# Optimization experiments

Hardware: AMD Instinct MI355X
Metric: run time of the kernel (lower is better)

Reference implementation:

```python
import jax, jax.numpy as jnp
import numpy as np

B, N, DIM = 32, 576, 1024
H, HD = 16, 64            # head_dim = DIM // H
M = HD * 2                # rand_feat_dim = head_dim * rand_feat_dim_ratio(2) = 128
LAM = 0.1
NUM_STEP = 10
SCALE = HD ** (-0.5)


def setup_inputs() -> dict:
    key = jax.random.key(0)
    ks = jax.random.split(key, 6)
    x = jax.random.normal(ks[0], (B, N, DIM), dtype=jnp.float32)
    qkv_w = jax.random.normal(ks[1], (2 * DIM, DIM), dtype=jnp.float32) * 0.02
    proj_w = jax.random.normal(ks[2], (DIM, DIM), dtype=jnp.float32) * 0.02
    proj_b = jnp.zeros((DIM,), dtype=jnp.float32)
    rand_matrix = jax.random.normal(ks[3], (H, HD, M), dtype=jnp.float32)
    kernel = jax.random.normal(ks[4], (1, H, N, M), dtype=jnp.float32)
    learned_k = jnp.eye(2 * M, dtype=jnp.float32)
    learned_lam = jnp.ones((1,), dtype=jnp.float32)
    learned_L = jnp.ones((1,), dtype=jnp.float32)
    return {"x": x, "qkv_w": qkv_w, "proj_w": proj_w, "proj_b": proj_b,
            "rand_matrix": rand_matrix, "kernel": kernel,
            "learned_k": learned_k, "learned_lam": learned_lam,
            "learned_L": learned_L}


def _soft_thresh(z, t):
    # torch: sign(z) * GELU(|z| - t), exact (erf) GELU
    return jnp.sign(z) * jax.nn.gelu(jnp.abs(z) - t, approximate=False)


def reference(x, qkv_w, proj_w, proj_b, rand_matrix, kernel,
              learned_k, learned_lam, learned_L):
    # qkv projection (no bias), split into q and v heads: [B,H,N,HD]
    qkv = (x @ qkv_w.T).reshape(B, N, 2, H, HD)
    q = jnp.transpose(qkv[:, :, 0], (0, 2, 1, 3))
    v = jnp.transpose(qkv[:, :, 1], (0, 2, 1, 3))

    # random-feature map (Performer-style positive features)
    q = q * SCALE ** 0.5
    logits = jnp.einsum('bhnd,hdm->bhnm', q, rand_matrix)
    sqnorm = 0.5 * jnp.sum(q * q, axis=-1, keepdims=True)
    phi = jnp.exp(logits - sqnorm) / (M ** 0.5)                 # [B,H,N,M]

    # concat learned kernel features, L2-normalize over token dim (dim=-2)
    q = jnp.concatenate([phi, jnp.broadcast_to(kernel, (B, H, N, M))], axis=-1)
    nrm = jnp.linalg.norm(q, axis=-2, keepdims=True)
    q = q / jnp.maximum(nrm, 1e-12)                              # [B,H,N,2M]

    kk = jnp.einsum('bhnp,bhnq->bhpq', q, q)                     # [B,H,2M,2M]
    inp = jnp.einsum('bhnp,bhnd->bhpd', q, v)                    # [B,H,2M,HD]

    # ISTA-like unrolled solver
    L = jax.lax.stop_gradient(
        jnp.max(jnp.sum(jnp.abs(kk), axis=-1), axis=-1))[..., None, None] + 1.0
    lam_learned = learned_lam * LAM                              # [1]
    eff_L = L / learned_L                                        # [B,H,1,1]
    kk_learned = jnp.einsum('pq,bhqr,rs->bhps', learned_k, kk, learned_k)

    z = _soft_thresh(inp, lam_learned)
    for _ in range(NUM_STEP):
        z = z - (jnp.einsum('bhpq,bhqd->bhpd', kk_learned, z) - inp) / eff_L
        z = _soft_thresh(z, lam_learned / eff_L)

    out = jnp.einsum('bhnp,bhpd->bhnd', q, z)                    # [B,H,N,HD]
    out = jnp.transpose(out, (0, 2, 1, 3)).reshape(B, N, DIM)
    return out @ proj_w.T + proj_b
```

## Files before the change

### kernel.cpp

```cpp
#include <hip/hip_runtime.h>
#include <math.h>

#define NN 576
#define LAMC 0.1f
#define NUM_STEP 10

typedef unsigned short u16;
typedef __attribute__((ext_vector_type(8))) short bf16x8;
typedef __attribute__((ext_vector_type(4))) float f32x4;

__device__ __forceinline__ float bf2f(u16 u) { return __uint_as_float(((unsigned)u) << 16); }
__device__ __forceinline__ u16 f2bf(float f) {
    unsigned x = __float_as_uint(f);
    return (u16)((x + 0x7fffu + ((x >> 16) & 1u)) >> 16);
}
__device__ __forceinline__ float soft_thresh(float z, float t) {
    float a = fabsf(z) - t;
    float g = 0.5f * a * (1.0f + erff(a * 0.70710678118654752f));
    float s = (z > 0.0f) ? 1.0f : ((z < 0.0f) ? -1.0f : 0.0f);
    return s * g;
}
__device__ __forceinline__ void gload16(const u16* g, const u16* l) {
    __builtin_amdgcn_global_load_lds(
        (const __attribute__((address_space(1))) unsigned int*)(g),
        (__attribute__((address_space(3))) unsigned int*)(l), 16, 0, 0);
}

__global__ __launch_bounds__(256) void k_cvt(const float* __restrict__ in,
                                             u16* __restrict__ out, int n4) {
    const int i = blockIdx.x * 256 + threadIdx.x;
    if (i >= n4) return;
    float4 v = reinterpret_cast<const float4*>(in)[i];
    ushort4 o;
    o.x = f2bf(v.x); o.y = f2bf(v.y); o.z = f2bf(v.z); o.w = f2bf(v.w);
    reinterpret_cast<ushort4*>(out)[i] = o;
}

__global__ __launch_bounds__(256) void k_cvtT(const float* __restrict__ Lk,
                                              u16* __restrict__ LkT) {
    const int r = blockIdx.x, s = threadIdx.x;
    LkT[r * 256 + s] = f2bf(Lk[s * 256 + r]);
}

__global__ __launch_bounds__(256) void k_randT(const float* __restrict__ rand_m,
                                               u16* __restrict__ randT) {
    const int i = blockIdx.x * 256 + threadIdx.x;
    const int h = i >> 13, rem = i & 8191;
    const int m = rem >> 6, d = rem & 63;
    randT[i] = f2bf(rand_m[(size_t)h * 8192 + d * 128 + m]);
}

__device__ __forceinline__ void nt128_body(const u16* __restrict__ A, const u16* __restrict__ B,
                                           const int K, u16 (&As)[128][32], u16 (&Bs)[128][32],
                                           f32x4 (&acc)[4][4]) {
    const int tid = threadIdx.x;
    const int lane = tid & 63, wid = tid >> 6;
    const int wr = (wid >> 1) * 64, wc = (wid & 1) * 64;
    const int fr = lane & 15, kg = lane >> 4;
    for (int k0 = 0; k0 < K; k0 += 32) {
        __syncthreads();
        #pragma unroll
        for (int c = 0; c < 2; ++c) {
            const int ch = wid + c * 4;
            gload16(&A[(size_t)(ch * 16 + (lane >> 2)) * K + k0 + (lane & 3) * 8], &As[ch * 16][0]);
            gload16(&B[(size_t)(ch * 16 + (lane >> 2)) * K + k0 + (lane & 3) * 8], &Bs[ch * 16][0]);
        }
        __syncthreads();
        bf16x8 af[4], bfr[4];
        #pragma unroll
        for (int i = 0; i < 4; ++i) af[i] = *reinterpret_cast<const bf16x8*>(&As[wr + i * 16 + fr][kg * 8]);
        #pragma unroll
        for (int j = 0; j < 4; ++j) bfr[j] = *reinterpret_cast<const bf16x8*>(&Bs[wc + j * 16 + fr][kg * 8]);
        #pragma unroll
        for (int i = 0; i < 4; ++i)
            #pragma unroll
            for (int j = 0; j < 4; ++j)
                acc[i][j] = __builtin_amdgcn_mfma_f32_16x16x32_bf16(af[i], bfr[j], acc[i][j], 0, 0, 0);
    }
}

__global__ __launch_bounds__(256) void k_qkv_mfma(const u16* __restrict__ A,
                                                  const u16* __restrict__ B,
                                                  u16* __restrict__ qbf,
                                                  u16* __restrict__ vT) {
    __shared__ u16 As[128][32];
    __shared__ u16 Bs[128][32];
    const int tid = threadIdx.x;
    const int wid = tid >> 6, lane = tid & 63;
    const int wr = (wid >> 1) * 64, wc = (wid & 1) * 64;
    const int lb = (blockIdx.x & 7) * 288 + (blockIdx.x >> 3);
    const int bm = lb >> 4, bn = lb & 15;
    const int row0 = bm * 128, col0 = bn * 128;
    const int fr = lane & 15, kg = lane >> 4;
    f32x4 acc[4][4];
    #pragma unroll
    for (int i = 0; i < 4; ++i)
        #pragma unroll
        for (int j = 0; j < 4; ++j) acc[i][j] = (f32x4){0.f, 0.f, 0.f, 0.f};
    nt128_body(A + (size_t)row0 * 1024, B + (size_t)col0 * 1024, 1024, As, Bs, acc);
    const bool isQ = (col0 < 1024);
    if (isQ) {
        const float qscale = 0.35355339059327373f;
        #pragma unroll
        for (int i = 0; i < 4; ++i) {
            #pragma unroll
            for (int r = 0; r < 4; ++r) {
                const int grow = row0 + wr + i * 16 + kg * 4 + r;
                const int b = grow / NN, n = grow % NN;
                #pragma unroll
                for (int j = 0; j < 4; ++j) {
                    const int gcol = col0 + wc + j * 16 + fr;
                    const int h = gcol >> 6, d = gcol & 63;
                    qbf[(((size_t)b * 16 + h) * NN + n) * 64 + d] = f2bf(acc[i][j][r] * qscale);
                }
            }
        }
    } else {
        #pragma unroll
        for (int i = 0; i < 4; ++i) {
            const int gb = row0 + wr + i * 16 + kg * 4;
            const int b = gb / NN, n = gb % NN;
            #pragma unroll
            for (int j = 0; j < 4; ++j) {
                const int c2 = col0 + wc + j * 16 + fr - 1024;
                const int h = c2 >> 6, d = c2 & 63;
                ushort4 pk;
                pk.x = f2bf(acc[i][j][0]); pk.y = f2bf(acc[i][j][1]);
                pk.z = f2bf(acc[i][j][2]); pk.w = f2bf(acc[i][j][3]);
                *reinterpret_cast<ushort4*>(&vT[(((size_t)b * 16 + h) * 64 + d) * 576 + n]) = pk;
            }
        }
    }
}

__global__ __launch_bounds__(256) void k_phi_mfma(const u16* __restrict__ qbf,
                                                  const u16* __restrict__ randT,
                                                  u16* __restrict__ phiT,
                                                  float* __restrict__ invn) {
    __shared__ u16 Rs[128][72];
    __shared__ u16 Qs[64][72];
    __shared__ u16 Ph[128][72];
    __shared__ float sn[64];
    __shared__ float snorm[256];
    const int bh = blockIdx.x, h = bh & 15;
    const int tid = threadIdx.x, lane = tid & 63, wid = tid >> 6;
    const int fr = lane & 15, kg = lane >> 4;
    #pragma unroll
    for (int c = 0; c < 4; ++c) {
        const int i = c * 256 + tid;
        const int m = i >> 3, k8 = (i & 7) * 8;
        *reinterpret_cast<uint4*>(&Rs[m][k8]) =
            *reinterpret_cast<const uint4*>(&randT[((size_t)h * 128 + m) * 64 + k8]);
    }
    const u16* Q = qbf + (size_t)bh * 576 * 64;
    const float invM = 0.08838834764831845f;
    float accs = 0.f;
    const int m2 = tid >> 1, c0 = (tid & 1) * 32;
    for (int nc = 0; nc < 9; ++nc) {
        const int n0 = nc * 64;
        __syncthreads();
        #pragma unroll
        for (int c = 0; c < 2; ++c) {
            const int i = c * 256 + tid;
            const int r = i >> 3, k8 = (i & 7) * 8;
            *reinterpret_cast<uint4*>(&Qs[r][k8]) =
                *reinterpret_cast<const uint4*>(&Q[(size_t)(n0 + r) * 64 + k8]);
        }
        __syncthreads();
        if (tid < 64) {
            float s = 0.f;
            #pragma unroll 8
            for (int d = 0; d < 64; ++d) { float v = bf2f(Qs[tid][d]); s = fmaf(v, v, s); }
            sn[tid] = 0.5f * s;
        }
        f32x4 acc[2][4];
        #pragma unroll
        for (int i = 0; i < 2; ++i)
            #pragma unroll
            for (int j = 0; j < 4; ++j) acc[i][j] = (f32x4){0.f, 0.f, 0.f, 0.f};
        #pragma unroll
        for (int ks = 0; ks < 2; ++ks) {
            bf16x8 af[2], bq[4];
            #pragma unroll
            for (int i = 0; i < 2; ++i)
                af[i] = *reinterpret_cast<const bf16x8*>(&Rs[wid * 32 + i * 16 + fr][ks * 32 + kg * 8]);
            #pragma unroll
            for (int j = 0; j < 4; ++j)
                bq[j] = *reinterpret_cast<const bf16x8*>(&Qs[j * 16 + fr][ks * 32 + kg * 8]);
            #pragma unroll
            for (int i = 0; i < 2; ++i)
                #pragma unroll
                for (int j = 0; j < 4; ++j)
                    acc[i][j] = __builtin_amdgcn_mfma_f32_16x16x32_bf16(af[i], bq[j], acc[i][j], 0, 0, 0);
        }
        __syncthreads();
        #pragma unroll
        for (int j = 0; j < 4; ++j) {
            const int n = j * 16 + fr;
            const float sv = sn[n];
            #pragma unroll
            for (int i = 0; i < 2; ++i) {
                #pragma unroll
                for (int r = 0; r < 4; ++r) {
                    const int m = wid * 32 + i * 16 + kg * 4 + r;
                    Ph[m][n] = f2bf(expf(acc[i][j][r] - sv) * invM);
                }
            }
        }
        __syncthreads();
        #pragma unroll
        for (int c = 0; c < 4; ++c) {
            const int i = c * 256 + tid;
            const int mm = i >> 3, k8 = (i & 7) * 8;
            *reinterpret_cast<uint4*>(&phiT[((size_t)bh * 128 + mm) * 576 + n0 + k8]) =
                *reinterpret_cast<const uint4*>(&Ph[mm][k8]);
        }
        {
            float s = 0.f;
            #pragma unroll 8
            for (int t = 0; t < 32; ++t) { float v = bf2f(Ph[m2][c0 + t]); s = fmaf(v, v, s); }
            accs += s;
        }
    }
    snorm[tid] = accs;
    __syncthreads();
    if (tid < 128)
        invn[bh * 128 + tid] = 1.0f / fmaxf(sqrtf(snorm[tid * 2] + snorm[tid * 2 + 1]), 1e-12f);
}

__global__ __launch_bounds__(128) void k_kernormT(const float* __restrict__ kern,
                                                  u16* __restrict__ kerT) {
    const int h = blockIdx.x, m = threadIdx.x;
    const float* kp = kern + (size_t)h * NN * 128 + m;
    float s = 0.f;
    for (int n = 0; n < NN; ++n) { float v = kp[(size_t)n * 128]; s = fmaf(v, v, s); }
    const float inv = 1.0f / fmaxf(sqrtf(s), 1e-12f);
    u16* op = kerT + ((size_t)h * 128 + m) * 576;
    for (int n = 0; n < NN; ++n) op[n] = f2bf(kp[(size_t)n * 128] * inv);
}

__global__ __launch_bounds__(512, 2) void k_gram_fat(const u16* __restrict__ phiT,
                                                     const u16* __restrict__ kerT,
                                                     const float* __restrict__ invn,
                                                     u16* __restrict__ kkb) {
    __shared__ u16 Qs[256][32];
    const int bh = blockIdx.x, h = bh & 15;
    const int tid = threadIdx.x, lane = tid & 63, wid = tid >> 6;
    const int wr = (wid & 3) * 64, wc = (wid >> 2) * 128;
    const int fr = lane & 15, kg = lane >> 4;
    const int lrow = lane >> 2;
    const int lslot = (lane & 3) ^ ((lane >> 3) & 3);
    f32x4 acc[4][8];
    #pragma unroll
    for (int i = 0; i < 4; ++i)
        #pragma unroll
        for (int j = 0; j < 8; ++j) acc[i][j] = (f32x4){0.f, 0.f, 0.f, 0.f};
    const int rslot = (kg ^ ((fr >> 1) & 3)) * 8;
    for (int k0 = 0; k0 < 576; k0 += 32) {
        __syncthreads();
        #pragma unroll
        for (int c = 0; c < 2; ++c) {
            const int chunk = wid * 2 + c;
            const int p = chunk * 16 + lrow;
            const u16* src = (p < 128)
                ? phiT + ((size_t)bh * 128 + p) * 576 + k0 + lslot * 8
                : kerT + ((size_t)h * 128 + (p - 128)) * 576 + k0 + lslot * 8;
            gload16(src, &Qs[chunk * 16][0]);
        }
        __syncthreads();
        bf16x8 af[4], bf[8];
        #pragma unroll
        for (int i = 0; i < 4; ++i) af[i] = *reinterpret_cast<const bf16x8*>(&Qs[wr + i * 16 + fr][rslot]);
        #pragma unroll
        for (int j = 0; j < 8; ++j) bf[j] = *reinterpret_cast<const bf16x8*>(&Qs[wc + j * 16 + fr][rslot]);
        #pragma unroll
        for (int i = 0; i < 4; ++i)
            #pragma unroll
            for (int j = 0; j < 8; ++j)
                acc[i][j] = __builtin_amdgcn_mfma_f32_16x16x32_bf16(af[i], bf[j], acc[i][j], 0, 0, 0);
    }
    const float* iv = invn + bh * 128;
    u16* C = kkb + (size_t)bh * 65536;
    float sq[8];
    #pragma unroll
    for (int j = 0; j < 8; ++j) { const int q = wc + j * 16 + fr; sq[j] = (q < 128) ? iv[q] : 1.0f; }
    #pragma unroll
    for (int i = 0; i < 4; ++i)
        #pragma unroll
        for (int rr = 0; rr < 4; ++rr) {
            const int p = wr + i * 16 + kg * 4 + rr;
            const float sp = (p < 128) ? iv[p] : 1.0f;
            #pragma unroll
            for (int j = 0; j < 8; ++j)
                C[(size_t)p * 256 + wc + j * 16 + fr] = f2bf(acc[i][j][rr] * sp * sq[j]);
        }
}

__global__ __launch_bounds__(512, 2) void k_lk_fat(const u16* __restrict__ Ab, size_t sA,
                                                   const u16* __restrict__ Bb, size_t sB,
                                                   u16* __restrict__ Cb) {
    __shared__ u16 As[256][32];
    __shared__ u16 Bs[256][32];
    const int idx = blockIdx.x;
    const int tid = threadIdx.x, lane = tid & 63, wid = tid >> 6;
    const int wr = (wid & 3) * 64, wc = (wid >> 2) * 128;
    const int fr = lane & 15, kg = lane >> 4;
    const int lrow = lane >> 2;
    const int lslot = (lane & 3) ^ ((lane >> 3) & 3);
    const u16* A = Ab + (size_t)idx * sA;
    const u16* B = Bb + (size_t)idx * sB;
    f32x4 acc[4][8];
    #pragma unroll
    for (int i = 0; i < 4; ++i)
        #pragma unroll
        for (int j = 0; j < 8; ++j) acc[i][j] = (f32x4){0.f, 0.f, 0.f, 0.f};
    const int rslot = (kg ^ ((fr >> 1) & 3)) * 8;
    for (int k0 = 0; k0 < 256; k0 += 32) {
        __syncthreads();
        #pragma unroll
        for (int c = 0; c < 2; ++c) {
            const int chunk = wid * 2 + c;
            const int p = chunk * 16 + lrow;
            gload16(&A[(size_t)p * 256 + k0 + lslot * 8], &As[chunk * 16][0]);
            gload16(&B[(size_t)p * 256 + k0 + lslot * 8], &Bs[chunk * 16][0]);
        }
        __syncthreads();
        bf16x8 af[4], bf[8];
        #pragma unroll
        for (int i = 0; i < 4; ++i) af[i] = *reinterpret_cast<const bf16x8*>(&As[wr + i * 16 + fr][rslot]);
        #pragma unroll
        for (int j = 0; j < 8; ++j) bf[j] = *reinterpret_cast<const bf16x8*>(&Bs[wc + j * 16 + fr][rslot]);
        #pragma unroll
        for (int i = 0; i < 4; ++i)
            #pragma unroll
            for (int j = 0; j < 8; ++j)
                acc[i][j] = __builtin_amdgcn_mfma_f32_16x16x32_bf16(af[i], bf[j], acc[i][j], 0, 0, 0);
    }
    u16* C = Cb + (size_t)idx * 65536;
    #pragma unroll
    for (int i = 0; i < 4; ++i)
        #pragma unroll
        for (int rr = 0; rr < 4; ++rr) {
            const int p = wr + i * 16 + kg * 4 + rr;
            #pragma unroll
            for (int j = 0; j < 8; ++j)
                C[(size_t)p * 256 + wc + j * 16 + fr] = f2bf(acc[i][j][rr]);
        }
}

__global__ __launch_bounds__(256) void k_inp_mfma(const u16* __restrict__ vT,
                                                  const u16* __restrict__ phiT,
                                                  const u16* __restrict__ kerT,
                                                  const float* __restrict__ invn,
                                                  float* __restrict__ inpT) {
    __shared__ u16 As[64][40];
    __shared__ u16 Bs[256][40];
    const int bh = blockIdx.x, h = bh & 15;
    const int tid = threadIdx.x, lane = tid & 63, wid = tid >> 6;
    const int fr = lane & 15, kg = lane >> 4;
    const u16* Av = vT + (size_t)bh * 64 * 576;
    f32x4 acc[4][4];
    #pragma unroll
    for (int i = 0; i < 4; ++i)
        #pragma unroll
        for (int j = 0; j < 4; ++j) acc[i][j] = (f32x4){0.f, 0.f, 0.f, 0.f};
    for (int k0 = 0; k0 < 576; k0 += 32) {
        __syncthreads();
        { const int r = tid >> 2, k8 = (tid & 3) * 8;
          *reinterpret_cast<uint4*>(&As[r][k8]) =
              *reinterpret_cast<const uint4*>(&Av[(size_t)r * 576 + k0 + k8]); }
        #pragma unroll
        for (int c = 0; c < 4; ++c) {
            const int q = c * 256 + tid;
            const int r = q >> 2, k8 = (q & 3) * 8;
            const u16* src = (r < 128) ? phiT + ((size_t)bh * 128 + r) * 576
                                       : kerT + ((size_t)h * 128 + (r - 128)) * 576;
            *reinterpret_cast<uint4*>(&Bs[r][k8]) =
                *reinterpret_cast<const uint4*>(&src[k0 + k8]);
        }
        __syncthreads();
        bf16x8 af[4], bfr[4];
        #pragma unroll
        for (int i = 0; i < 4; ++i) af[i] = *reinterpret_cast<const bf16x8*>(&As[i * 16 + fr][kg * 8]);
        #pragma unroll
        for (int j = 0; j < 4; ++j) bfr[j] = *reinterpret_cast<const bf16x8*>(&Bs[wid * 64 + j * 16 + fr][kg * 8]);
        #pragma unroll
        for (int i = 0; i < 4; ++i)
            #pragma unroll
            for (int j = 0; j < 4; ++j)
                acc[i][j] = __builtin_amdgcn_mfma_f32_16x16x32_bf16(af[i], bfr[j], acc[i][j], 0, 0, 0);
    }
    float* O = inpT + (size_t)bh * 16384;
    float sc[4];
    #pragma unroll
    for (int j = 0; j < 4; ++j) {
        const int p = wid * 64 + j * 16 + fr;
        sc[j] = (p < 128) ? invn[bh * 128 + p] : 1.0f;
    }
    #pragma unroll
    for (int i = 0; i < 4; ++i)
        #pragma unroll
        for (int r = 0; r < 4; ++r)
            #pragma unroll
            for (int j = 0; j < 4; ++j)
                O[(size_t)(i * 16 + kg * 4 + r) * 256 + wid * 64 + j * 16 + fr] = acc[i][j][r] * sc[j];
}

__global__ __launch_bounds__(256) void k_L(const u16* __restrict__ kkb,
                                           const float* __restrict__ lL,
                                           float* __restrict__ effL) {
    const int bh = blockIdx.x;
    const u16* row = kkb + (size_t)bh * 65536 + (size_t)threadIdx.x * 256;
    float s = 0.f;
    for (int q = 0; q < 256; ++q) s += fabsf(bf2f(row[q]));
    __shared__ float red[256];
    red[threadIdx.x] = s;
    __syncthreads();
    for (int st = 128; st > 0; st >>= 1) {
        if (threadIdx.x < st) red[threadIdx.x] = fmaxf(red[threadIdx.x], red[threadIdx.x + st]);
        __syncthreads();
    }
    if (threadIdx.x == 0) effL[bh] = (red[0] + 1.0f) / lL[0];
}

__global__ __launch_bounds__(256) void k_ista_reg(const u16* __restrict__ kkl,
                                                  const float* __restrict__ inpT,
                                                  u16* __restrict__ zbf,
                                                  const float* __restrict__ effL,
                                                  const float* __restrict__ llam) {
    __shared__ u16 zs[32][256];
    const int bh = blockIdx.x >> 1, dh = blockIdx.x & 1;
    const int tid = threadIdx.x, lane = tid & 63, wid = tid >> 6;
    const int wr = wid * 64;
    const int fr = lane & 15, kg = lane >> 4;
    const u16* Kk = kkl + (size_t)bh * 65536;
    bf16x8 af[4][8];
    #pragma unroll
    for (int i = 0; i < 4; ++i) {
        const int p = wr + i * 16 + fr;
        #pragma unroll
        for (int c = 0; c < 8; ++c)
            af[i][c] = *reinterpret_cast<const bf16x8*>(&Kk[(size_t)p * 256 + c * 32 + kg * 8]);
    }
    const float* I = inpT + (size_t)bh * 16384 + (size_t)dh * 32 * 256;
    const float invL = 1.0f / effL[bh];
    const float lam = llam[0] * LAMC;
    const float thr = lam * invL;
    float4 ip[4][2];
    #pragma unroll
    for (int i = 0; i < 4; ++i) {
        const int pb = wr + i * 16 + kg * 4;
        #pragma unroll
        for (int j = 0; j < 2; ++j) {
            const int d = j * 16 + fr;
            ip[i][j] = *reinterpret_cast<const float4*>(&I[(size_t)d * 256 + pb]);
            const int pc = pb ^ ((d & 7) << 3);
            ushort4 pk;
            pk.x = f2bf(soft_thresh(ip[i][j].x, lam));
            pk.y = f2bf(soft_thresh(ip[i][j].y, lam));
            pk.z = f2bf(soft_thresh(ip[i][j].z, lam));
            pk.w = f2bf(soft_thresh(ip[i][j].w, lam));
            *reinterpret_cast<ushort4*>(&zs[d][pc]) = pk;
        }
    }
    __syncthreads();
    for (int step = 0; step < NUM_STEP; ++step) {
        f32x4 acc[4][2];
        #pragma unroll
        for (int i = 0; i < 4; ++i)
            #pragma unroll
            for (int j = 0; j < 2; ++j) acc[i][j] = (f32x4){0.f, 0.f, 0.f, 0.f};
        #pragma unroll
        for (int c = 0; c < 8; ++c) {
            bf16x8 bz[2];
            #pragma unroll
            for (int j = 0; j < 2; ++j) {
                const int d = j * 16 + fr;
                bz[j] = *reinterpret_cast<const bf16x8*>(&zs[d][(c * 32 + kg * 8) ^ ((d & 7) << 3)]);
            }
            #pragma unroll
            for (int i = 0; i < 4; ++i)
                #pragma unroll
                for (int j = 0; j < 2; ++j)
                    acc[i][j] = __builtin_amdgcn_mfma_f32_16x16x32_bf16(af[i][c], bz[j], acc[i][j], 0, 0, 0);
        }
        __syncthreads();
        #pragma unroll
        for (int i = 0; i < 4; ++i) {
            const int pb = wr + i * 16 + kg * 4;
            #pragma unroll
            for (int j = 0; j < 2; ++j) {
                const int d = j * 16 + fr;
                const int pc = pb ^ ((d & 7) << 3);
                ushort4 zo = *reinterpret_cast<const ushort4*>(&zs[d][pc]);
                ushort4 pk;
                pk.x = f2bf(soft_thresh(bf2f(zo.x) - (acc[i][j][0] - ip[i][j].x) * invL, thr));
                pk.y = f2bf(soft_thresh(bf2f(zo.y) - (acc[i][j][1] - ip[i][j].y) * invL, thr));
                pk.z = f2bf(soft_thresh(bf2f(zo.z) - (acc[i][j][2] - ip[i][j].z) * invL, thr));
                pk.w = f2bf(soft_thresh(bf2f(zo.w) - (acc[i][j][3] - ip[i][j].w) * invL, thr));
                *reinterpret_cast<ushort4*>(&zs[d][pc]) = pk;
            }
        }
        __syncthreads();
    }
    u16* Z = zbf + (size_t)bh * 16384 + (size_t)dh * 32 * 256;
    #pragma unroll
    for (int c = 0; c < 4; ++c) {
        const int i = c * 256 + tid;
        const int d = i >> 5, p8 = (i & 31) * 8;
        *reinterpret_cast<uint4*>(&Z[(size_t)d * 256 + p8]) =
            *reinterpret_cast<const uint4*>(&zs[d][p8 ^ ((d & 7) << 3)]);
    }
}

__global__ __launch_bounds__(256) void k_outpre_mfma(const u16* __restrict__ phiT,
                                                     const u16* __restrict__ kerT,
                                                     const u16* __restrict__ zbf,
                                                     const float* __restrict__ invn,
                                                     u16* __restrict__ outp) {
    __shared__ u16 Zs[64][264];
    __shared__ u16 Qt[64][264];
    __shared__ u16 Os[64][72];
    const int bh = blockIdx.x, b = bh >> 4, h = bh & 15;
    const int tid = threadIdx.x, lane = tid & 63, wid = tid >> 6;
    const int fr = lane & 15, kg = lane >> 4;
    const u16* Z = zbf + (size_t)bh * 16384;
    #pragma unroll
    for (int c = 0; c < 8; ++c) {
        const int i = c * 256 + tid;
        const int d = i >> 5, k8 = (i & 31) * 8;
        uint4 v = *reinterpret_cast<const uint4*>(&Z[(size_t)d * 256 + k8]);
        if (k8 < 128) {
            const float4 s0 = *reinterpret_cast<const float4*>(&invn[bh * 128 + k8]);
            const float4 s1 = *reinterpret_cast<const float4*>(&invn[bh * 128 + k8 + 4]);
            uint4 o;
            o.x = (unsigned)f2bf(__uint_as_float(v.x << 16) * s0.x) |
                  ((unsigned)f2bf(__uint_as_float(v.x & 0xffff0000u) * s0.y) << 16);
            o.y = (unsigned)f2bf(__uint_as_float(v.y << 16) * s0.z) |
                  ((unsigned)f2bf(__uint_as_float(v.y & 0xffff0000u) * s0.w) << 16);
            o.z = (unsigned)f2bf(__uint_as_float(v.z << 16) * s1.x) |
                  ((unsigned)f2bf(__uint_as_float(v.z & 0xffff0000u) * s1.y) << 16);
            o.w = (unsigned)f2bf(__uint_as_float(v.w << 16) * s1.z) |
                  ((unsigned)f2bf(__uint_as_float(v.w & 0xffff0000u) * s1.w) << 16);
            v = o;
        }
        *reinterpret_cast<uint4*>(&Zs[d][k8]) = v;
    }
    for (int nc = 0; nc < 9; ++nc) {
        const int n0 = nc * 64;
        __syncthreads();
        #pragma unroll
        for (int c = 0; c < 8; ++c) {
            const int i = c * 256 + tid;
            const int p = i >> 3, j8 = (i & 7) * 8;
            const u16* src = (p < 128) ? &phiT[((size_t)bh * 128 + p) * 576 + n0 + j8]
                                       : &kerT[((size_t)h * 128 + (p - 128)) * 576 + n0 + j8];
            uint4 v = *reinterpret_cast<const uint4*>(src);
            Qt[j8 + 0][p] = (u16)(v.x & 0xffffu); Qt[j8 + 1][p] = (u16)(v.x >> 16);
            Qt[j8 + 2][p] = (u16)(v.y & 0xffffu); Qt[j8 + 3][p] = (u16)(v.y >> 16);
            Qt[j8 + 4][p] = (u16)(v.z & 0xffffu); Qt[j8 + 5][p] = (u16)(v.z >> 16);
            Qt[j8 + 6][p] = (u16)(v.w & 0xffffu); Qt[j8 + 7][p] = (u16)(v.w >> 16);
        }
        __syncthreads();
        f32x4 acc[4];
        #pragma unroll
        for (int j = 0; j < 4; ++j) acc[j] = (f32x4){0.f, 0.f, 0.f, 0.f};
        #pragma unroll
        for (int ks = 0; ks < 8; ++ks) {
            bf16x8 aq = *reinterpret_cast<const bf16x8*>(&Qt[wid * 16 + fr][ks * 32 + kg * 8]);
            #pragma unroll
            for (int j = 0; j < 4; ++j) {
                bf16x8 bz = *reinterpret_cast<const bf16x8*>(&Zs[j * 16 + fr][ks * 32 + kg * 8]);
                acc[j] = __builtin_amdgcn_mfma_f32_16x16x32_bf16(aq, bz, acc[j], 0, 0, 0);
            }
        }
        __syncthreads();
        #pragma unroll
        for (int j = 0; j < 4; ++j)
            #pragma unroll
            for (int r = 0; r < 4; ++r)
                Os[wid * 16 + kg * 4 + r][j * 16 + fr] = f2bf(acc[j][r]);
        __syncthreads();
        #pragma unroll
        for (int c = 0; c < 2; ++c) {
            const int i = c * 256 + tid;
            const int nn = i >> 3, k8 = (i & 7) * 8;
            *reinterpret_cast<uint4*>(&outp[((size_t)b * NN + n0 + nn) * 1024 + h * 64 + k8]) =
                *reinterpret_cast<const uint4*>(&Os[nn][k8]);
        }
    }
}

__global__ __launch_bounds__(256) void k_proj_mfma(const u16* __restrict__ A,
                                                   const u16* __restrict__ B,
                                                   const float* __restrict__ bias,
                                                   float* __restrict__ out) {
    __shared__ u16 As[128][32];
    __shared__ u16 Bs[128][32];
    const int tid = threadIdx.x;
    const int wid = tid >> 6, lane = tid & 63;
    const int wr = (wid >> 1) * 64, wc = (wid & 1) * 64;
    const int lb = (blockIdx.x & 7) * 144 + (blockIdx.x >> 3);
    const int bm = lb >> 3, bn = lb & 7;
    const int row0 = bm * 128, col0 = bn * 128;
    const int fr = lane & 15, kg = lane >> 4;
    f32x4 acc[4][4];
    #pragma unroll
    for (int i = 0; i < 4; ++i)
        #pragma unroll
        for (int j = 0; j < 4; ++j) acc[i][j] = (f32x4){0.f, 0.f, 0.f, 0.f};
    nt128_body(A + (size_t)row0 * 1024, B + (size_t)col0 * 1024, 1024, As, Bs, acc);
    #pragma unroll
    for (int i = 0; i < 4; ++i)
        #pragma unroll
        for (int r = 0; r < 4; ++r) {
            const int grow = row0 + wr + i * 16 + kg * 4 + r;
            #pragma unroll
            for (int j = 0; j < 4; ++j) {
                const int gcol = col0 + wc + j * 16 + fr;
                out[(size_t)grow * 1024 + gcol] = acc[i][j][r] + bias[gcol];
            }
        }
}

extern "C" void kernel_launch(void* const* d_in, const int* in_sizes, int n_in,
                              void* d_out, int out_size, void* d_ws, size_t ws_size,
                              hipStream_t stream) {
    const float* x      = (const float*)d_in[0];
    const float* qkv_w  = (const float*)d_in[1];
    const float* proj_w = (const float*)d_in[2];
    const float* proj_b = (const float*)d_in[3];
    const float* rand_m = (const float*)d_in[4];
    const float* kern   = (const float*)d_in[5];
    const float* Lk     = (const float*)d_in[6];
    const float* llam   = (const float*)d_in[7];
    const float* lL     = (const float*)d_in[8];
    float* out = (float*)d_out;

    const size_t NEED = 248514560ull;
    if (ws_size < NEED) { hipMemsetAsync(d_out, 0, (size_t)out_size * 4, stream); return; }
    char* base = (char*)d_ws;
    u16*   pwb  = (u16*)  (base + 0);
    float* effL = (float*)(base + 2097152);
    u16*   Lkb  = (u16*)  (base + 2099200);
    u16*   LkTb = (u16*)  (base + 2230272);
    u16*   kerT = (u16*)  (base + 2361344);
    u16*   randT= (u16*)  (base + 4720640);
    u16*   phiT = (u16*)  (base + 4982784);
    u16*   kkb  = (u16*)  (base + 80480256);
    float* inpT = (float*)(base + 147589120);
    u16*   zbf  = (u16*)  (base + 181143552);
    float* invn = (float*)(base + 248252416);
    u16*   vT   = (u16*)  (base + 80480256);
    u16*   wb   = (u16*)  (base + 118228992);
    u16*   qbf  = (u16*)  (base + 147589120);
    u16*   xb   = (u16*)  (base + 197920768);
    u16*   tmpb = (u16*)  (base + 181143552);
    u16*   outp = (u16*)  (base + 80480256);

    k_cvt        <<<18432, 256, 0, stream>>>(x, xb, 4718592);
    k_cvt        <<<2048,  256, 0, stream>>>(qkv_w, wb, 524288);
    k_cvt        <<<1024,  256, 0, stream>>>(proj_w, pwb, 262144);
    k_cvt        <<<64,    256, 0, stream>>>(Lk, Lkb, 16384);
    k_cvtT       <<<256,   256, 0, stream>>>(Lk, LkTb);
    k_randT      <<<512,   256, 0, stream>>>(rand_m, randT);
    k_kernormT   <<<16,    128, 0, stream>>>(kern, kerT);
    k_qkv_mfma   <<<2304,  256, 0, stream>>>(xb, wb, qbf, vT);
    k_phi_mfma   <<<512,   256, 0, stream>>>(qbf, randT, phiT, invn);
    k_inp_mfma   <<<512,   256, 0, stream>>>(vT, phiT, kerT, invn, inpT);
    k_gram_fat   <<<512,   512, 0, stream>>>(phiT, kerT, invn, kkb);
    k_L          <<<512,   256, 0, stream>>>(kkb, lL, effL);
    k_lk_fat     <<<512,   512, 0, stream>>>(Lkb, 0, kkb, 65536, tmpb);
    k_lk_fat     <<<512,   512, 0, stream>>>(tmpb, 65536, LkTb, 0, kkb);
    k_ista_reg   <<<1024,  256, 0, stream>>>(kkb, inpT, zbf, effL, llam);
    k_outpre_mfma<<<512,   256, 0, stream>>>(phiT, kerT, zbf, invn, outp);
    k_proj_mfma  <<<1152,  256, 0, stream>>>(outp, pwb, proj_b, out);
}
```

Before: 610.0 us.

## Use 256x256 tiles with swizzled LDS for qkv and proj GEMMs

Replaces the 128x128-tile, 256-thread GEMM kernels for the qkv and output projections with 256x256-tile, 512-thread kernels where each wave computes a 64x128 sub-tile. LDS reads and writes now use an XOR swizzle on the k-slot to avoid bank conflicts. This is meant to raise arithmetic intensity and cut global/LDS traffic per MFMA. In exchange it uses more registers and launches fewer blocks (576 and 288), so load balance across CUs may suffer.

```diff
diff --git a/kernel.cpp b/kernel.cpp
--- a/kernel.cpp
+++ b/kernel.cpp
@@ -50,54 +50,49 @@
     randT[i] = f2bf(rand_m[(size_t)h * 8192 + d * 128 + m]);
 }
 
-__device__ __forceinline__ void nt128_body(const u16* __restrict__ A, const u16* __restrict__ B,
-                                           const int K, u16 (&As)[128][32], u16 (&Bs)[128][32],
-                                           f32x4 (&acc)[4][4]) {
-    const int tid = threadIdx.x;
-    const int lane = tid & 63, wid = tid >> 6;
-    const int wr = (wid >> 1) * 64, wc = (wid & 1) * 64;
-    const int fr = lane & 15, kg = lane >> 4;
-    for (int k0 = 0; k0 < K; k0 += 32) {
+__global__ __launch_bounds__(512, 2) void k_qkv_fat(const u16* __restrict__ A,
+                                                    const u16* __restrict__ B,
+                                                    u16* __restrict__ qbf,
+                                                    u16* __restrict__ vT) {
+    __shared__ u16 As[256][32];
+    __shared__ u16 Bs[256][32];
+    const int tid = threadIdx.x, lane = tid & 63, wid = tid >> 6;
+    const int wr = (wid & 3) * 64, wc = (wid >> 2) * 128;
+    const int fr = lane & 15, kg = lane >> 4;
+    const int lrow = lane >> 2;
+    const int lslot = (lane & 3) ^ ((lane >> 3) & 3);
+    const int lb = (blockIdx.x & 7) * 72 + (blockIdx.x >> 3);
+    const int bm = lb >> 3, bn = lb & 7;
+    const int row0 = bm * 256, col0 = bn * 256;
+    const u16* Ab = A + (size_t)row0 * 1024;
+    const u16* Bb = B + (size_t)col0 * 1024;
+    f32x4 acc[4][8];
+    #pragma unroll
+    for (int i = 0; i < 4; ++i)
+        #pragma unroll
+        for (int j = 0; j < 8; ++j) acc[i][j] = (f32x4){0.f, 0.f, 0.f, 0.f};
+    const int rslot = (kg ^ ((fr >> 1) & 3)) * 8;
+    for (int k0 = 0; k0 < 1024; k0 += 32) {
         __syncthreads();
         #pragma unroll
         for (int c = 0; c < 2; ++c) {
-            const int ch = wid + c * 4;
-            gload16(&A[(size_t)(ch * 16 + (lane >> 2)) * K + k0 + (lane & 3) * 8], &As[ch * 16][0]);
-            gload16(&B[(size_t)(ch * 16 + (lane >> 2)) * K + k0 + (lane & 3) * 8], &Bs[ch * 16][0]);
-        }
-        __syncthreads();
-        bf16x8 af[4], bfr[4];
-        #pragma unroll
-        for (int i = 0; i < 4; ++i) af[i] = *reinterpret_cast<const bf16x8*>(&As[wr + i * 16 + fr][kg * 8]);
-        #pragma unroll
-        for (int j = 0; j < 4; ++j) bfr[j] = *reinterpret_cast<const bf16x8*>(&Bs[wc + j * 16 + fr][kg * 8]);
+            const int chunk = wid * 2 + c;
+            const int p = chunk * 16 + lrow;
+            gload16(&Ab[(size_t)p * 1024 + k0 + lslot * 8], &As[chunk * 16][0]);
+            gload16(&Bb[(size_t)p * 1024 + k0 + lslot * 8], &Bs[chunk * 16][0]);
+        }
+        __syncthreads();
+        bf16x8 af[4], bf[8];
+        #pragma unroll
+        for (int i = 0; i < 4; ++i) af[i] = *reinterpret_cast<const bf16x8*>(&As[wr + i * 16 + fr][rslot]);
+        #pragma unroll
+        for (int j = 0; j < 8; ++j) bf[j] = *reinterpret_cast<const bf16x8*>(&Bs[wc + j * 16 + fr][rslot]);
         #pragma unroll
         for (int i = 0; i < 4; ++i)
             #pragma unroll
-            for (int j = 0; j < 4; ++j)
-                acc[i][j] = __builtin_amdgcn_mfma_f32_16x16x32_bf16(af[i], bfr[j], acc[i][j], 0, 0, 0);
-    }
-}
-
-__global__ __launch_bounds__(256) void k_qkv_mfma(const u16* __restrict__ A,
-                                                  const u16* __restrict__ B,
-                                                  u16* __restrict__ qbf,
-                                                  u16* __restrict__ vT) {
-    __shared__ u16 As[128][32];
-    __shared__ u16 Bs[128][32];
-    const int tid = threadIdx.x;
-    const int wid = tid >> 6, lane = tid & 63;
-    const int wr = (wid >> 1) * 64, wc = (wid & 1) * 64;
-    const int lb = (blockIdx.x & 7) * 288 + (blockIdx.x >> 3);
-    const int bm = lb >> 4, bn = lb & 15;
-    const int row0 = bm * 128, col0 = bn * 128;
-    const int fr = lane & 15, kg = lane >> 4;
-    f32x4 acc[4][4];
-    #pragma unroll
-    for (int i = 0; i < 4; ++i)
-        #pragma unroll
-        for (int j = 0; j < 4; ++j) acc[i][j] = (f32x4){0.f, 0.f, 0.f, 0.f};
-    nt128_body(A + (size_t)row0 * 1024, B + (size_t)col0 * 1024, 1024, As, Bs, acc);
+            for (int j = 0; j < 8; ++j)
+                acc[i][j] = __builtin_amdgcn_mfma_f32_16x16x32_bf16(af[i], bf[j], acc[i][j], 0, 0, 0);
+    }
     const bool isQ = (col0 < 1024);
     if (isQ) {
         const float qscale = 0.35355339059327373f;
@@ -108,7 +103,7 @@
                 const int grow = row0 + wr + i * 16 + kg * 4 + r;
                 const int b = grow / NN, n = grow % NN;
                 #pragma unroll
-                for (int j = 0; j < 4; ++j) {
+                for (int j = 0; j < 8; ++j) {
                     const int gcol = col0 + wc + j * 16 + fr;
                     const int h = gcol >> 6, d = gcol & 63;
                     qbf[(((size_t)b * 16 + h) * NN + n) * 64 + d] = f2bf(acc[i][j][r] * qscale);
@@ -121,7 +116,7 @@
             const int gb = row0 + wr + i * 16 + kg * 4;
             const int b = gb / NN, n = gb % NN;
             #pragma unroll
-            for (int j = 0; j < 4; ++j) {
+            for (int j = 0; j < 8; ++j) {
                 const int c2 = col0 + wc + j * 16 + fr - 1024;
                 const int h = c2 >> 6, d = c2 & 63;
                 ushort4 pk;
@@ -591,32 +586,56 @@
     }
 }
 
-__global__ __launch_bounds__(256) void k_proj_mfma(const u16* __restrict__ A,
-                                                   const u16* __restrict__ B,
-                                                   const float* __restrict__ bias,
-                                                   float* __restrict__ out) {
-    __shared__ u16 As[128][32];
-    __shared__ u16 Bs[128][32];
-    const int tid = threadIdx.x;
-    const int wid = tid >> 6, lane = tid & 63;
-    const int wr = (wid >> 1) * 64, wc = (wid & 1) * 64;
-    const int lb = (blockIdx.x & 7) * 144 + (blockIdx.x >> 3);
-    const int bm = lb >> 3, bn = lb & 7;
-    const int row0 = bm * 128, col0 = bn * 128;
-    const int fr = lane & 15, kg = lane >> 4;
-    f32x4 acc[4][4];
-    #pragma unroll
-    for (int i = 0; i < 4; ++i)
-        #pragma unroll
-        for (int j = 0; j < 4; ++j) acc[i][j] = (f32x4){0.f, 0.f, 0.f, 0.f};
-    nt128_body(A + (size_t)row0 * 1024, B + (size_t)col0 * 1024, 1024, As, Bs, acc);
+__global__ __launch_bounds__(512, 2) void k_proj_fat(const u16* __restrict__ A,
+                                                     const u16* __restrict__ B,
+                                                     const float* __restrict__ bias,
+                                                     float* __restrict__ out) {
+    __shared__ u16 As[256][32];
+    __shared__ u16 Bs[256][32];
+    const int tid = threadIdx.x, lane = tid & 63, wid = tid >> 6;
+    const int wr = (wid & 3) * 64, wc = (wid >> 2) * 128;
+    const int fr = lane & 15, kg = lane >> 4;
+    const int lrow = lane >> 2;
+    const int lslot = (lane & 3) ^ ((lane >> 3) & 3);
+    const int lb = (blockIdx.x & 7) * 36 + (blockIdx.x >> 3);
+    const int bm = lb >> 2, bn = lb & 3;
+    const int row0 = bm * 256, col0 = bn * 256;
+    const u16* Ab = A + (size_t)row0 * 1024;
+    const u16* Bb = B + (size_t)col0 * 1024;
+    f32x4 acc[4][8];
+    #pragma unroll
+    for (int i = 0; i < 4; ++i)
+        #pragma unroll
+        for (int j = 0; j < 8; ++j) acc[i][j] = (f32x4){0.f, 0.f, 0.f, 0.f};
+    const int rslot = (kg ^ ((fr >> 1) & 3)) * 8;
+    for (int k0 = 0; k0 < 1024; k0 += 32) {
+        __syncthreads();
+        #pragma unroll
+        for (int c = 0; c < 2; ++c) {
+            const int chunk = wid * 2 + c;
+            const int p = chunk * 16 + lrow;
+            gload16(&Ab[(size_t)p * 1024 + k0 + lslot * 8], &As[chunk * 16][0]);
+            gload16(&Bb[(size_t)p * 1024 + k0 + lslot * 8], &Bs[chunk * 16][0]);
+        }
+        __syncthreads();
+        bf16x8 af[4], bf[8];
+        #pragma unroll
+        for (int i = 0; i < 4; ++i) af[i] = *reinterpret_cast<const bf16x8*>(&As[wr + i * 16 + fr][rslot]);
+        #pragma unroll
+        for (int j = 0; j < 8; ++j) bf[j] = *reinterpret_cast<const bf16x8*>(&Bs[wc + j * 16 + fr][rslot]);
+        #pragma unroll
+        for (int i = 0; i < 4; ++i)
+            #pragma unroll
+            for (int j = 0; j < 8; ++j)
+                acc[i][j] = __builtin_amdgcn_mfma_f32_16x16x32_bf16(af[i], bf[j], acc[i][j], 0, 0, 0);
+    }
     #pragma unroll
     for (int i = 0; i < 4; ++i)
         #pragma unroll
         for (int r = 0; r < 4; ++r) {
             const int grow = row0 + wr + i * 16 + kg * 4 + r;
             #pragma unroll
-            for (int j = 0; j < 4; ++j) {
+            for (int j = 0; j < 8; ++j) {
                 const int gcol = col0 + wc + j * 16 + fr;
                 out[(size_t)grow * 1024 + gcol] = acc[i][j][r] + bias[gcol];
             }
@@ -665,7 +684,7 @@
     k_cvtT       <<<256,   256, 0, stream>>>(Lk, LkTb);
     k_randT      <<<512,   256, 0, stream>>>(rand_m, randT);
     k_kernormT   <<<16,    128, 0, stream>>>(kern, kerT);
-    k_qkv_mfma   <<<2304,  256, 0, stream>>>(xb, wb, qbf, vT);
+    k_qkv_fat    <<<576,   512, 0, stream>>>(xb, wb, qbf, vT);
     k_phi_mfma   <<<512,   256, 0, stream>>>(qbf, randT, phiT, invn);
     k_inp_mfma   <<<512,   256, 0, stream>>>(vT, phiT, kerT, invn, inpT);
     k_gram_fat   <<<512,   512, 0, stream>>>(phiT, kerT, invn, kkb);
@@ -674,5 +693,5 @@
     k_lk_fat     <<<512,   512, 0, stream>>>(tmpb, 65536, LkTb, 0, kkb);
     k_ista_reg   <<<1024,  256, 0, stream>>>(kkb, inpT, zbf, effL, llam);
     k_outpre_mfma<<<512,   256, 0, stream>>>(phiT, kerT, zbf, invn, outp);
-    k_proj_mfma  <<<1152,  256, 0, stream>>>(outp, pwb, proj_b, out);
-}
+    k_proj_fat   <<<288,   512, 0, stream>>>(outp, pwb, proj_b, out);
+}
```

Result: slower. 647.2 us (+6.1%).

## Merge prep conversion kernels and fuse row-abs-sum reduction into gram epilogue

Applied to the files above, without the earlier changes.

Six small weight and parameter conversion launches are merged into one block-indexed prep kernel to cut launch overhead. The separate k_L kernel, which re-read the whole bf16 gram matrix to compute the max row abs-sum, is removed. That reduction is now done in the gram kernel's epilogue with wave shuffles and a shared-memory max. The abs-sum now uses the fp32 values before bf16 rounding, which slightly changes eff_L, and the gram kernel uses more shared memory and more barriers.

```diff
diff --git a/kernel.cpp b/kernel.cpp
--- a/kernel.cpp
+++ b/kernel.cpp
@@ -36,18 +36,52 @@
     reinterpret_cast<ushort4*>(out)[i] = o;
 }
 
-__global__ __launch_bounds__(256) void k_cvtT(const float* __restrict__ Lk,
-                                              u16* __restrict__ LkT) {
-    const int r = blockIdx.x, s = threadIdx.x;
-    LkT[r * 256 + s] = f2bf(Lk[s * 256 + r]);
-}
-
-__global__ __launch_bounds__(256) void k_randT(const float* __restrict__ rand_m,
-                                               u16* __restrict__ randT) {
-    const int i = blockIdx.x * 256 + threadIdx.x;
-    const int h = i >> 13, rem = i & 8191;
-    const int m = rem >> 6, d = rem & 63;
-    randT[i] = f2bf(rand_m[(size_t)h * 8192 + d * 128 + m]);
+__global__ __launch_bounds__(256) void k_prep(const float* __restrict__ qkv_w,
+                                              const float* __restrict__ proj_w,
+                                              const float* __restrict__ Lk,
+                                              const float* __restrict__ rand_m,
+                                              const float* __restrict__ kern,
+                                              u16* __restrict__ wb,
+                                              u16* __restrict__ pwb,
+                                              u16* __restrict__ Lkb,
+                                              u16* __restrict__ LkTb,
+                                              u16* __restrict__ randT,
+                                              u16* __restrict__ kerT) {
+    const int b = blockIdx.x;
+    if (b < 2048) {
+        const int i = b * 256 + threadIdx.x;
+        float4 v = reinterpret_cast<const float4*>(qkv_w)[i];
+        ushort4 o; o.x = f2bf(v.x); o.y = f2bf(v.y); o.z = f2bf(v.z); o.w = f2bf(v.w);
+        reinterpret_cast<ushort4*>(wb)[i] = o;
+    } else if (b < 3072) {
+        const int i = (b - 2048) * 256 + threadIdx.x;
+        float4 v = reinterpret_cast<const float4*>(proj_w)[i];
+        ushort4 o; o.x = f2bf(v.x); o.y = f2bf(v.y); o.z = f2bf(v.z); o.w = f2bf(v.w);
+        reinterpret_cast<ushort4*>(pwb)[i] = o;
+    } else if (b < 3136) {
+        const int i = (b - 3072) * 256 + threadIdx.x;
+        float4 v = reinterpret_cast<const float4*>(Lk)[i];
+        ushort4 o; o.x = f2bf(v.x); o.y = f2bf(v.y); o.z = f2bf(v.z); o.w = f2bf(v.w);
+        reinterpret_cast<ushort4*>(Lkb)[i] = o;
+    } else if (b < 3392) {
+        const int r = b - 3136, s = threadIdx.x;
+        LkTb[r * 256 + s] = f2bf(Lk[s * 256 + r]);
+    } else if (b < 3904) {
+        const int i = (b - 3392) * 256 + threadIdx.x;
+        const int h = i >> 13, rem = i & 8191;
+        const int m = rem >> 6, d = rem & 63;
+        randT[i] = f2bf(rand_m[(size_t)h * 8192 + d * 128 + m]);
+    } else {
+        const int h = b - 3904, m = threadIdx.x;
+        if (m < 128) {
+            const float* kp = kern + (size_t)h * NN * 128 + m;
+            float s = 0.f;
+            for (int n = 0; n < NN; ++n) { float v = kp[(size_t)n * 128]; s = fmaf(v, v, s); }
+            const float inv = 1.0f / fmaxf(sqrtf(s), 1e-12f);
+            u16* op = kerT + ((size_t)h * 128 + m) * 576;
+            for (int n = 0; n < NN; ++n) op[n] = f2bf(kp[(size_t)n * 128] * inv);
+        }
+    }
 }
 
 __device__ __forceinline__ void nt128_body(const u16* __restrict__ A, const u16* __restrict__ B,
@@ -228,22 +262,15 @@
         invn[bh * 128 + tid] = 1.0f / fmaxf(sqrtf(snorm[tid * 2] + snorm[tid * 2 + 1]), 1e-12f);
 }
 
-__global__ __launch_bounds__(128) void k_kernormT(const float* __restrict__ kern,
-                                                  u16* __restrict__ kerT) {
-    const int h = blockIdx.x, m = threadIdx.x;
-    const float* kp = kern + (size_t)h * NN * 128 + m;
-    float s = 0.f;
-    for (int n = 0; n < NN; ++n) { float v = kp[(size_t)n * 128]; s = fmaf(v, v, s); }
-    const float inv = 1.0f / fmaxf(sqrtf(s), 1e-12f);
-    u16* op = kerT + ((size_t)h * 128 + m) * 576;
-    for (int n = 0; n < NN; ++n) op[n] = f2bf(kp[(size_t)n * 128] * inv);
-}
-
 __global__ __launch_bounds__(512, 2) void k_gram_fat(const u16* __restrict__ phiT,
                                                      const u16* __restrict__ kerT,
                                                      const float* __restrict__ invn,
-                                                     u16* __restrict__ kkb) {
+                                                     const float* __restrict__ lL,
+                                                     u16* __restrict__ kkb,
+                                                     float* __restrict__ effL) {
     __shared__ u16 Qs[256][32];
+    __shared__ float rs2[2][256];
+    __shared__ float red[256];
     const int bh = blockIdx.x, h = bh & 15;
     const int tid = threadIdx.x, lane = tid & 63, wid = tid >> 6;
     const int wr = (wid & 3) * 64, wc = (wid >> 2) * 128;
@@ -290,10 +317,25 @@
         for (int rr = 0; rr < 4; ++rr) {
             const int p = wr + i * 16 + kg * 4 + rr;
             const float sp = (p < 128) ? iv[p] : 1.0f;
-            #pragma unroll
-            for (int j = 0; j < 8; ++j)
-                C[(size_t)p * 256 + wc + j * 16 + fr] = f2bf(acc[i][j][rr] * sp * sq[j]);
-        }
+            float rsum = 0.f;
+            #pragma unroll
+            for (int j = 0; j < 8; ++j) {
+                const float val = acc[i][j][rr] * sp * sq[j];
+                C[(size_t)p * 256 + wc + j * 16 + fr] = f2bf(val);
+                rsum += fabsf(val);
+            }
+            #pragma unroll
+            for (int mk = 1; mk < 16; mk <<= 1) rsum += __shfl_xor(rsum, mk);
+            if (fr == 0) rs2[wid >> 2][p] = rsum;
+        }
+    __syncthreads();
+    if (tid < 256) red[tid] = rs2[0][tid] + rs2[1][tid];
+    __syncthreads();
+    for (int st = 128; st > 0; st >>= 1) {
+        if (tid < st) red[tid] = fmaxf(red[tid], red[tid + st]);
+        __syncthreads();
+    }
+    if (tid == 0) effL[bh] = (red[0] + 1.0f) / lL[0];
 }
 
 __global__ __launch_bounds__(512, 2) void k_lk_fat(const u16* __restrict__ Ab, size_t sA,
@@ -404,23 +446,6 @@
             #pragma unroll
             for (int j = 0; j < 4; ++j)
                 O[(size_t)(i * 16 + kg * 4 + r) * 256 + wid * 64 + j * 16 + fr] = acc[i][j][r] * sc[j];
-}
-
-__global__ __launch_bounds__(256) void k_L(const u16* __restrict__ kkb,
-                                           const float* __restrict__ lL,
-                                           float* __restrict__ effL) {
-    const int bh = blockIdx.x;
-    const u16* row = kkb + (size_t)bh * 65536 + (size_t)threadIdx.x * 256;
-    float s = 0.f;
-    for (int q = 0; q < 256; ++q) s += fabsf(bf2f(row[q]));
-    __shared__ float red[256];
-    red[threadIdx.x] = s;
-    __syncthreads();
-    for (int st = 128; st > 0; st >>= 1) {
-        if (threadIdx.x < st) red[threadIdx.x] = fmaxf(red[threadIdx.x], red[threadIdx.x + st]);
-        __syncthreads();
-    }
-    if (threadIdx.x == 0) effL[bh] = (red[0] + 1.0f) / lL[0];
 }
 
 __global__ __launch_bounds__(256) void k_ista_reg(const u16* __restrict__ kkl,
@@ -659,17 +684,12 @@
     u16*   outp = (u16*)  (base + 80480256);
 
     k_cvt        <<<18432, 256, 0, stream>>>(x, xb, 4718592);
-    k_cvt        <<<2048,  256, 0, stream>>>(qkv_w, wb, 524288);
-    k_cvt        <<<1024,  256, 0, stream>>>(proj_w, pwb, 262144);
-    k_cvt        <<<64,    256, 0, stream>>>(Lk, Lkb, 16384);
-    k_cvtT       <<<256,   256, 0, stream>>>(Lk, LkTb);
-    k_randT      <<<512,   256, 0, stream>>>(rand_m, randT);
-    k_kernormT   <<<16,    128, 0, stream>>>(kern, kerT);
+    k_prep       <<<3920,  256, 0, stream>>>(qkv_w, proj_w, Lk, rand_m, kern,
+                                             wb, pwb, Lkb, LkTb, randT, kerT);
     k_qkv_mfma   <<<2304,  256, 0, stream>>>(xb, wb, qbf, vT);
     k_phi_mfma   <<<512,   256, 0, stream>>>(qbf, randT, phiT, invn);
     k_inp_mfma   <<<512,   256, 0, stream>>>(vT, phiT, kerT, invn, inpT);
-    k_gram_fat   <<<512,   512, 0, stream>>>(phiT, kerT, invn, kkb);
-    k_L          <<<512,   256, 0, stream>>>(kkb, lL, effL);
+    k_gram_fat   <<<512,   512, 0, stream>>>(phiT, kerT, invn, lL, kkb, effL);
     k_lk_fat     <<<512,   512, 0, stream>>>(Lkb, 0, kkb, 65536, tmpb);
     k_lk_fat     <<<512,   512, 0, stream>>>(tmpb, 65536, LkTb, 0, kkb);
     k_ista_reg   <<<1024,  256, 0, stream>>>(kkb, inpT, zbf, effL, llam);
```

New measurement: 587.7 us. -3.7%, faster.
